# Performance work log

Measured on AMD Instinct MI355X. Metric: run time of the kernel, lower is better.

Reference implementation:

```python
import jax, jax.numpy as jnp
import numpy as np

N_NODES = 50000
N_EDGES = 800000
NFEAT, NHID, ZDIM = 256, 128, 32
N_PAIRS = 10000


def spmm(row, col, val, h, n):
    # sparse adj (COO) @ dense h : gather source rows, scale, segment-sum into dest rows
    return jax.ops.segment_sum(val[:, None] * h[col], row, num_segments=n)


def setup_inputs() -> dict:
    key = jax.random.key(0)
    ks = jax.random.split(key, 16)
    features = jax.random.normal(ks[0], (N_NODES, NFEAT), dtype=jnp.float32)
    adj_row = jnp.sort(jax.random.randint(ks[1], (N_EDGES,), 0, N_NODES, dtype=jnp.int32))
    adj_col = jax.random.randint(ks[2], (N_EDGES,), 0, N_NODES, dtype=jnp.int32)
    adj_val = jax.random.uniform(ks[3], (N_EDGES,), dtype=jnp.float32)
    idx = jax.random.randint(ks[4], (2, N_PAIRS), 0, N_NODES, dtype=jnp.int32)
    sc = lambda fan: 1.0 / np.sqrt(fan)
    W0 = jax.random.normal(ks[5], (NFEAT, NHID), dtype=jnp.float32) * sc(NFEAT)
    b0 = jnp.zeros((NHID,), jnp.float32)
    W1 = jax.random.normal(ks[6], (NHID, NHID), dtype=jnp.float32) * sc(NHID)
    b1 = jnp.zeros((NHID,), jnp.float32)
    W2 = jax.random.normal(ks[7], (NHID, NHID), dtype=jnp.float32) * sc(NHID)
    b2 = jnp.zeros((NHID,), jnp.float32)
    bil_w = jax.random.normal(ks[8], (ZDIM, NHID, NHID), dtype=jnp.float32) * sc(NHID)
    bil_b = jnp.zeros((ZDIM,), jnp.float32)
    dw1 = jax.random.normal(ks[9], (ZDIM, ZDIM), dtype=jnp.float32) * sc(ZDIM)
    db1 = jnp.zeros((ZDIM,), jnp.float32)
    dw2 = jax.random.normal(ks[10], (ZDIM, 1), dtype=jnp.float32) * sc(ZDIM)
    db2 = jnp.zeros((1,), jnp.float32)
    return dict(features=features, adj_row=adj_row, adj_col=adj_col, adj_val=adj_val,
                idx=idx, W0=W0, b0=b0, W1=W1, b1=b1, W2=W2, b2=b2,
                bil_w=bil_w, bil_b=bil_b, dw1=dw1, db1=db1, dw2=dw2, db2=db2)


def reference(features, adj_row, adj_col, adj_val, idx,
              W0, b0, W1, b1, W2, b2, bil_w, bil_b, dw1, db1, dw2, db2):
    n = features.shape[0]
    # encode: stacked GCN layers (Kipf: relu(adj @ (x @ W) + b)), residual from layer 1 on
    x = jax.nn.relu(spmm(adj_row, adj_col, adj_val, features @ W0, n) + b0)
    res = x
    x = jax.nn.relu(spmm(adj_row, adj_col, adj_val, x @ W1, n) + b1) + res
    res = x
    x = jax.nn.relu(spmm(adj_row, adj_col, adj_val, x @ W2, n) + b2) + res
    latent = x  # dropout p=0.0 -> identity
    # decode: bilinear on node pairs, ELU, 2-layer MLP
    a = latent[idx[0]]  # [P, NHID]
    b = latent[idx[1]]  # [P, NHID]
    feat = jax.nn.elu(jnp.einsum('pd,kde,pe->pk', a, bil_w, b) + bil_b)
    h = jax.nn.elu(feat @ dw1 + db1)
    predictions = h @ dw2 + db2  # [P, 1]
    return predictions, latent
```

## Files before the change

### kernel.cpp

```cpp
#include <hip/hip_runtime.h>
#include <hip/hip_bf16.h>
#include <math.h>

#define N_NODES 50000
#define N_EDGES 800000
#define NFEAT   256
#define NHID    128
#define ZDIM    32
#define N_PAIRS 10000

typedef __attribute__((ext_vector_type(8))) short bf16x8;
typedef __attribute__((ext_vector_type(4))) float f32x4;

__global__ void k_build_row_ptr(const int* __restrict__ row, int* __restrict__ row_ptr) {
    int e = blockIdx.x * blockDim.x + threadIdx.x;
    if (e >= N_EDGES) return;
    int cur  = row[e];
    int prev = (e == 0) ? -1 : row[e - 1];
    for (int r = prev + 1; r <= cur; ++r) row_ptr[r] = e;
    if (e == N_EDGES - 1) {
        for (int r = cur + 1; r <= N_NODES; ++r) row_ptr[r] = N_EDGES;
    }
}

__global__ __launch_bounds__(256) void k_pack_gw(const float* __restrict__ W,
                                                 __hip_bfloat16* __restrict__ wpk) {
    int i  = blockIdx.x * 256 + threadIdx.x;
    int j  = i & 7;
    int l  = (i >> 3) & 63;
    int n  = (i >> 9) & 7;
    int kk = i >> 12;
    int d  = kk * 32 + (l >> 4) * 8 + j;
    int e  = n * 16 + (l & 15);
    wpk[i] = __float2bfloat16(W[(long)d * 128 + e]);
}

__global__ __launch_bounds__(256) void k_pack_w2(const float* __restrict__ bw,
                                                 __hip_bfloat16* __restrict__ wh,
                                                 __hip_bfloat16* __restrict__ wl) {
    int i  = blockIdx.x * 256 + threadIdx.x;
    int j  = i & 7;
    int l  = (i >> 3) & 63;
    int n  = (i >> 9) & 7;
    int kk = (i >> 12) & 3;
    int k  = i >> 14;
    int d  = kk * 32 + (l >> 4) * 8 + j;
    int e  = n * 16 + (l & 15);
    float w = bw[((long)k * 128 + d) * 128 + e];
    __hip_bfloat16 h = __float2bfloat16(w);
    wh[i] = h;
    wl[i] = __float2bfloat16(w - __bfloat162float(h));
}

template <int K>
__global__ __launch_bounds__(256) void k_gemm_mfma(const float* __restrict__ X,
                                                   const __hip_bfloat16* __restrict__ wpk,
                                                   float* __restrict__ Y) {
    const int PAD = 8;
    __shared__ __hip_bfloat16 as[64][K + PAD];
    const int tid = threadIdx.x;
    const long r0 = (long)blockIdx.x * 64;

    const int QK = K / 4;
    for (int i = tid; i < 64 * QK; i += 256) {
        int row = i / QK, q = i - row * QK;
        float4 v = make_float4(0.f, 0.f, 0.f, 0.f);
        if (r0 + row < N_NODES)
            v = *reinterpret_cast<const float4*>(&X[(r0 + row) * (long)K + q * 4]);
        as[row][q * 4 + 0] = __float2bfloat16(v.x);
        as[row][q * 4 + 1] = __float2bfloat16(v.y);
        as[row][q * 4 + 2] = __float2bfloat16(v.z);
        as[row][q * 4 + 3] = __float2bfloat16(v.w);
    }
    __syncthreads();

    const int wrow = (tid >> 6) * 16;
    const int lane = tid & 63;
    const int l15  = lane & 15, l4 = lane >> 4;

    bf16x8 af[K / 32];
#pragma unroll
    for (int kk = 0; kk < K / 32; ++kk)
        af[kk] = *reinterpret_cast<const bf16x8*>(&as[wrow + l15][kk * 32 + l4 * 8]);

    f32x4 acc[8];
#pragma unroll
    for (int n = 0; n < 8; ++n) acc[n] = (f32x4){0.f, 0.f, 0.f, 0.f};

#pragma unroll 2
    for (int n = 0; n < 8; ++n) {
        f32x4 a = {0.f, 0.f, 0.f, 0.f};
#pragma unroll
        for (int kk = 0; kk < K / 32; ++kk) {
            bf16x8 wf = *reinterpret_cast<const bf16x8*>(&wpk[(((kk * 8 + n) * 64) + lane) * 8]);
            a = __builtin_amdgcn_mfma_f32_16x16x32_bf16(af[kk], wf, a, 0, 0, 0);
        }
        acc[n] = a;
    }

#pragma unroll
    for (int n = 0; n < 8; ++n)
#pragma unroll
        for (int q = 0; q < 4; ++q) {
            long row = r0 + wrow + l4 * 4 + q;
            if (row < N_NODES) Y[row * 128 + n * 16 + l15] = acc[n][q];
        }
}

template <bool HAS_RES>
__global__ __launch_bounds__(256) void k_spmm_post(const float* __restrict__ H,
                                                   const int* __restrict__ row_ptr,
                                                   const int* __restrict__ col,
                                                   const float* __restrict__ val,
                                                   const float* __restrict__ bias,
                                                   const float* __restrict__ res,
                                                   float* __restrict__ out) {
    const int w    = threadIdx.x >> 6;
    const int lane = threadIdx.x & 63;
    const int r    = blockIdx.x * 4 + w;
    if (r >= N_NODES) return;
    const int e0 = row_ptr[r], e1 = row_ptr[r + 1];
    const float2* H2 = reinterpret_cast<const float2*>(H);

    float2 acc = make_float2(0.f, 0.f);
    for (int base = e0; base < e1; base += 64) {
        int n = e1 - base; if (n > 64) n = 64;
        float v = 0.f; int c = 0;
        if (lane < n) { v = val[base + lane]; c = col[base + lane]; }
#pragma unroll 2
        for (int i = 0; i < n; ++i) {
            float vi = __shfl(v, i);
            int   ci = __shfl(c, i);
            float2 h = H2[(long)ci * 64 + lane];
            acc.x += vi * h.x;
            acc.y += vi * h.y;
        }
    }

    float2 bv = reinterpret_cast<const float2*>(bias)[lane];
    acc.x = fmaxf(acc.x + bv.x, 0.f);
    acc.y = fmaxf(acc.y + bv.y, 0.f);
    if (HAS_RES) {
        float2 rv = reinterpret_cast<const float2*>(res)[(long)r * 64 + lane];
        acc.x += rv.x; acc.y += rv.y;
    }
    reinterpret_cast<float2*>(out)[(long)r * 64 + lane] = acc;
}

__global__ __launch_bounds__(512, 4) void k_bilinear_mfma(const float* __restrict__ latent,
                                                          const int* __restrict__ idx0,
                                                          const int* __restrict__ idx1,
                                                          const __hip_bfloat16* __restrict__ wpk_hi,
                                                          const __hip_bfloat16* __restrict__ wpk_lo,
                                                          const float* __restrict__ bb,
                                                          const float* __restrict__ dw1,
                                                          const float* __restrict__ db1,
                                                          const float* __restrict__ dw2,
                                                          const float* __restrict__ db2,
                                                          float* __restrict__ pred) {
    __shared__ __hip_bfloat16 ah[32][136];
    __shared__ __hip_bfloat16 al[32][136];
    __shared__ float          bs[32][132];
    __shared__ float          fl[ZDIM][32];
    const int p0  = blockIdx.x * 32;
    const int tid = threadIdx.x;

    for (int i = tid; i < 32 * 32; i += 512) {
        int p = i >> 5, q = i & 31;
        int pi = p0 + p; if (pi >= N_PAIRS) pi = N_PAIRS - 1;
        const float4 av = *reinterpret_cast<const float4*>(&latent[(long)idx0[pi] * 128 + q * 4]);
        const float4 bv = *reinterpret_cast<const float4*>(&latent[(long)idx1[pi] * 128 + q * 4]);
        float a4[4] = {av.x, av.y, av.z, av.w};
#pragma unroll
        for (int t = 0; t < 4; ++t) {
            __hip_bfloat16 h = __float2bfloat16(a4[t]);
            ah[p][q * 4 + t] = h;
            al[p][q * 4 + t] = __float2bfloat16(a4[t] - __bfloat162float(h));
        }
        *reinterpret_cast<float4*>(&bs[p][q * 4]) = bv;
    }
    __syncthreads();

    const int wave = tid >> 6;
    const int lane = tid & 63;
    const int l15  = lane & 15, l4 = lane >> 4;

    bf16x8 af[2][4];
#pragma unroll
    for (int M = 0; M < 2; ++M)
#pragma unroll
        for (int kk = 0; kk < 4; ++kk)
            af[M][kk] = *reinterpret_cast<const bf16x8*>(&ah[M * 16 + l15][kk * 32 + l4 * 8]);

#pragma unroll 1
    for (int k2 = 0; k2 < 4; ++k2) {
        const int k = wave * 4 + k2;
        float fsum[2][4];
#pragma unroll
        for (int M = 0; M < 2; ++M)
#pragma unroll
            for (int q = 0; q < 4; ++q) fsum[M][q] = 0.f;

#pragma unroll 1
        for (int n = 0; n < 8; ++n) {
            f32x4 acc0 = {0.f, 0.f, 0.f, 0.f};
            f32x4 acc1 = {0.f, 0.f, 0.f, 0.f};
#pragma unroll
            for (int kk = 0; kk < 4; ++kk) {
                const long ci = (((long)(k * 4 + kk) * 8 + n) * 512) + lane * 8;
                bf16x8 wh = *reinterpret_cast<const bf16x8*>(&wpk_hi[ci]);
                bf16x8 wl = *reinterpret_cast<const bf16x8*>(&wpk_lo[ci]);
                bf16x8 a0l = *reinterpret_cast<const bf16x8*>(&al[l15][kk * 32 + l4 * 8]);
                bf16x8 a1l = *reinterpret_cast<const bf16x8*>(&al[16 + l15][kk * 32 + l4 * 8]);
                acc0 = __builtin_amdgcn_mfma_f32_16x16x32_bf16(af[0][kk], wh, acc0, 0, 0, 0);
                acc0 = __builtin_amdgcn_mfma_f32_16x16x32_bf16(af[0][kk], wl, acc0, 0, 0, 0);
                acc0 = __builtin_amdgcn_mfma_f32_16x16x32_bf16(a0l,      wh, acc0, 0, 0, 0);
                acc1 = __builtin_amdgcn_mfma_f32_16x16x32_bf16(af[1][kk], wh, acc1, 0, 0, 0);
                acc1 = __builtin_amdgcn_mfma_f32_16x16x32_bf16(af[1][kk], wl, acc1, 0, 0, 0);
                acc1 = __builtin_amdgcn_mfma_f32_16x16x32_bf16(a1l,      wh, acc1, 0, 0, 0);
            }
#pragma unroll
            for (int q = 0; q < 4; ++q) {
                fsum[0][q] += acc0[q] * bs[l4 * 4 + q][n * 16 + l15];
                fsum[1][q] += acc1[q] * bs[16 + l4 * 4 + q][n * 16 + l15];
            }
        }

#pragma unroll
        for (int M = 0; M < 2; ++M) {
            float v0 = fsum[M][0], v1 = fsum[M][1], v2 = fsum[M][2], v3 = fsum[M][3];
#pragma unroll
            for (int off = 1; off < 16; off <<= 1) {
                v0 += __shfl_xor(v0, off);
                v1 += __shfl_xor(v1, off);
                v2 += __shfl_xor(v2, off);
                v3 += __shfl_xor(v3, off);
            }
            if (l15 == 0) {
                const float bbk = bb[k];
                float vv[4] = {v0, v1, v2, v3};
#pragma unroll
                for (int q = 0; q < 4; ++q) {
                    float v = vv[q] + bbk;
                    fl[k][M * 16 + l4 * 4 + q] = (v > 0.f) ? v : (expf(v) - 1.f);
                }
            }
        }
    }
    __syncthreads();

    if (tid < 32) {
        int p = p0 + tid;
        if (p < N_PAIRS) {
            float f[ZDIM];
#pragma unroll
            for (int k = 0; k < ZDIM; ++k) f[k] = fl[k][tid];
            float acc = db2[0];
            for (int j = 0; j < ZDIM; ++j) {
                float h = db1[j];
#pragma unroll
                for (int k = 0; k < ZDIM; ++k) h += f[k] * dw1[k * ZDIM + j];
                h = (h > 0.f) ? h : (expf(h) - 1.f);
                acc += h * dw2[j];
            }
            pred[p] = acc;
        }
    }
}

extern "C" void kernel_launch(void* const* d_in, const int* in_sizes, int n_in,
                              void* d_out, int out_size, void* d_ws, size_t ws_size,
                              hipStream_t stream) {
    const float* features = (const float*)d_in[0];
    const int*   adj_row  = (const int*)d_in[1];
    const int*   adj_col  = (const int*)d_in[2];
    const float* adj_val  = (const float*)d_in[3];
    const int*   idx      = (const int*)d_in[4];
    const float* W0 = (const float*)d_in[5];
    const float* b0 = (const float*)d_in[6];
    const float* W1 = (const float*)d_in[7];
    const float* b1 = (const float*)d_in[8];
    const float* W2 = (const float*)d_in[9];
    const float* b2 = (const float*)d_in[10];
    const float* bil_w = (const float*)d_in[11];
    const float* bil_b = (const float*)d_in[12];
    const float* dw1 = (const float*)d_in[13];
    const float* db1 = (const float*)d_in[14];
    const float* dw2 = (const float*)d_in[15];
    const float* db2 = (const float*)d_in[16];

    float* pred   = (float*)d_out;
    float* latent = (float*)d_out + N_PAIRS;

    char* ws = (char*)d_ws;
    float* xw   = (float*)ws;                                 ws += (size_t)N_NODES * NHID * 4;
    float* xcur = (float*)ws;                                 ws += (size_t)N_NODES * NHID * 4;
    int*   row_ptr = (int*)ws;                                ws += (size_t)(N_NODES + 1) * 4;
    __hip_bfloat16* wpk_hi = (__hip_bfloat16*)ws;             ws += (size_t)ZDIM * NHID * NHID * 2;
    __hip_bfloat16* wpk_lo = (__hip_bfloat16*)ws;             ws += (size_t)ZDIM * NHID * NHID * 2;
    __hip_bfloat16* w0pk = (__hip_bfloat16*)ws;               ws += (size_t)NFEAT * NHID * 2;
    __hip_bfloat16* w1pk = (__hip_bfloat16*)ws;               ws += (size_t)NHID * NHID * 2;
    __hip_bfloat16* w2pk = (__hip_bfloat16*)ws;               ws += (size_t)NHID * NHID * 2;

    const int*  idx0 = idx;
    const int*  idx1 = idx + N_PAIRS;

    k_build_row_ptr<<<(N_EDGES + 255) / 256, 256, 0, stream>>>(adj_row, row_ptr);
    k_pack_w2<<<(ZDIM * NHID * NHID) / 256, 256, 0, stream>>>(bil_w, wpk_hi, wpk_lo);
    k_pack_gw<<<(NFEAT * NHID) / 256, 256, 0, stream>>>(W0, w0pk);
    k_pack_gw<<<(NHID * NHID) / 256, 256, 0, stream>>>(W1, w1pk);
    k_pack_gw<<<(NHID * NHID) / 256, 256, 0, stream>>>(W2, w2pk);

    const int GB  = (N_NODES + 63) / 64;
    const int SB  = (N_NODES + 3) / 4;

    k_gemm_mfma<NFEAT><<<GB, 256, 0, stream>>>(features, w0pk, xw);
    k_spmm_post<false><<<SB, 256, 0, stream>>>(xw, row_ptr, adj_col, adj_val, b0, nullptr, xcur);

    k_gemm_mfma<NHID><<<GB, 256, 0, stream>>>(xcur, w1pk, xw);
    k_spmm_post<true><<<SB, 256, 0, stream>>>(xw, row_ptr, adj_col, adj_val, b1, xcur, xcur);

    k_gemm_mfma<NHID><<<GB, 256, 0, stream>>>(xcur, w2pk, xw);
    k_spmm_post<true><<<SB, 256, 0, stream>>>(xw, row_ptr, adj_col, adj_val, b2, xcur, latent);

    k_bilinear_mfma<<<(N_PAIRS + 31) / 32, 512, 0, stream>>>(latent, idx0, idx1, wpk_hi, wpk_lo,
                                                             bil_b, dw1, db1, dw2, db2, pred);
}
```

Before: 431.2 us.

## Split SpMM across 16-feature slices with four edges per wave in parallel

The SpMM kernel is restructured. Each launch now uses a 2D grid whose y dimension picks one of 8 feature slices of 16 floats. Within a wave, four groups of 16 lanes each process a different edge at the same time, and the partial sums are combined with xor shuffles before the bias, ReLU and residual epilogue. The aim is more parallelism and more gathers in flight per row. The cost is 8x more blocks, edge metadata re-read once per slice, and narrower 64-byte gather segments. A 12-byte workspace pad is also added after row_ptr, which looks like an alignment adjustment for the packed weight buffers.

Result: slower. 729.3 us (+69.1%).

```diff
diff --git a/kernel.cpp b/kernel.cpp
--- a/kernel.cpp
+++ b/kernel.cpp
@@ -108,43 +108,44 @@
 }
 
 template <bool HAS_RES>
-__global__ __launch_bounds__(256) void k_spmm_post(const float* __restrict__ H,
-                                                   const int* __restrict__ row_ptr,
-                                                   const int* __restrict__ col,
-                                                   const float* __restrict__ val,
-                                                   const float* __restrict__ bias,
-                                                   const float* __restrict__ res,
-                                                   float* __restrict__ out) {
+__global__ __launch_bounds__(256) void k_spmm_slice(const float* __restrict__ H,
+                                                    const int* __restrict__ row_ptr,
+                                                    const int* __restrict__ col,
+                                                    const float* __restrict__ val,
+                                                    const float* __restrict__ bias,
+                                                    const float* __restrict__ res,
+                                                    float* __restrict__ out) {
     const int w    = threadIdx.x >> 6;
     const int lane = threadIdx.x & 63;
     const int r    = blockIdx.x * 4 + w;
+    const int s    = blockIdx.y;
     if (r >= N_NODES) return;
+    const int g = lane >> 4;
+    const int j = lane & 15;
     const int e0 = row_ptr[r], e1 = row_ptr[r + 1];
-    const float2* H2 = reinterpret_cast<const float2*>(H);
-
-    float2 acc = make_float2(0.f, 0.f);
+
+    float acc = 0.f;
     for (int base = e0; base < e1; base += 64) {
         int n = e1 - base; if (n > 64) n = 64;
         float v = 0.f; int c = 0;
         if (lane < n) { v = val[base + lane]; c = col[base + lane]; }
-#pragma unroll 2
-        for (int i = 0; i < n; ++i) {
+        const int nn = (n + 3) >> 2;
+        for (int u = 0; u < nn; ++u) {
+            int i = u * 4 + g;
             float vi = __shfl(v, i);
             int   ci = __shfl(c, i);
-            float2 h = H2[(long)ci * 64 + lane];
-            acc.x += vi * h.x;
-            acc.y += vi * h.y;
-        }
-    }
-
-    float2 bv = reinterpret_cast<const float2*>(bias)[lane];
-    acc.x = fmaxf(acc.x + bv.x, 0.f);
-    acc.y = fmaxf(acc.y + bv.y, 0.f);
-    if (HAS_RES) {
-        float2 rv = reinterpret_cast<const float2*>(res)[(long)r * 64 + lane];
-        acc.x += rv.x; acc.y += rv.y;
-    }
-    reinterpret_cast<float2*>(out)[(long)r * 64 + lane] = acc;
+            acc += vi * H[(long)ci * 128 + s * 16 + j];
+        }
+    }
+    acc += __shfl_xor(acc, 16);
+    acc += __shfl_xor(acc, 32);
+
+    if (g == 0) {
+        const int f = s * 16 + j;
+        acc = fmaxf(acc + bias[f], 0.f);
+        if (HAS_RES) acc += res[(long)r * 128 + f];
+        out[(long)r * 128 + f] = acc;
+    }
 }
 
 __global__ __launch_bounds__(512, 4) void k_bilinear_mfma(const float* __restrict__ latent,
@@ -296,6 +297,7 @@
     float* xw   = (float*)ws;                                 ws += (size_t)N_NODES * NHID * 4;
     float* xcur = (float*)ws;                                 ws += (size_t)N_NODES * NHID * 4;
     int*   row_ptr = (int*)ws;                                ws += (size_t)(N_NODES + 1) * 4;
+    ws += 12;
     __hip_bfloat16* wpk_hi = (__hip_bfloat16*)ws;             ws += (size_t)ZDIM * NHID * NHID * 2;
     __hip_bfloat16* wpk_lo = (__hip_bfloat16*)ws;             ws += (size_t)ZDIM * NHID * NHID * 2;
     __hip_bfloat16* w0pk = (__hip_bfloat16*)ws;               ws += (size_t)NFEAT * NHID * 2;
@@ -312,16 +314,16 @@
     k_pack_gw<<<(NHID * NHID) / 256, 256, 0, stream>>>(W2, w2pk);
 
     const int GB  = (N_NODES + 63) / 64;
-    const int SB  = (N_NODES + 3) / 4;
+    const dim3 SB((N_NODES + 3) / 4, 8);
 
     k_gemm_mfma<NFEAT><<<GB, 256, 0, stream>>>(features, w0pk, xw);
-    k_spmm_post<false><<<SB, 256, 0, stream>>>(xw, row_ptr, adj_col, adj_val, b0, nullptr, xcur);
+    k_spmm_slice<false><<<SB, 256, 0, stream>>>(xw, row_ptr, adj_col, adj_val, b0, nullptr, xcur);
 
     k_gemm_mfma<NHID><<<GB, 256, 0, stream>>>(xcur, w1pk, xw);
-    k_spmm_post<true><<<SB, 256, 0, stream>>>(xw, row_ptr, adj_col, adj_val, b1, xcur, xcur);
+    k_spmm_slice<true><<<SB, 256, 0, stream>>>(xw, row_ptr, adj_col, adj_val, b1, xcur, xcur);
 
     k_gemm_mfma<NHID><<<GB, 256, 0, stream>>>(xcur, w2pk, xw);
-    k_spmm_post<true><<<SB, 256, 0, stream>>>(xw, row_ptr, adj_col, adj_val, b2, xcur, latent);
+    k_spmm_slice<true><<<SB, 256, 0, stream>>>(xw, row_ptr, adj_col, adj_val, b2, xcur, latent);
 
     k_bilinear_mfma<<<(N_PAIRS + 31) / 32, 512, 0, stream>>>(latent, idx0, idx1, wpk_hi, wpk_lo,
                                                              bil_b, dw1, db1, dw2, db2, pred);
```
